# Performance work log

Hardware: AMD Instinct MI355X
Metric: run time of the kernel (lower is better)

## Reference

```python
import jax, jax.numpy as jnp
import numpy as np


def setup_inputs() -> dict:
    key = jax.random.key(0)
    k1, k2 = jax.random.split(key)
    # x: (N, width, T) with width == emb_width
    x = jax.random.normal(k1, (16, 64, 8192), dtype=jnp.float32)
    # codebook k: (k_bins, emb_width)
    k = jax.random.normal(k2, (2048, 64), dtype=jnp.float32) * 0.02
    return {"x": x, "k": k}


def reference(x, k):
    N, width, T = x.shape
    # preprocess: (N, width, T) -> (N*T, width)
    xf = jnp.transpose(x, (0, 2, 1)).reshape(-1, width)
    n_el = xf.size  # static python int
    prenorm = jnp.linalg.norm(xf - jnp.mean(xf)) / np.sqrt(n_el)
    # quantise: pairwise squared distances to codebook, argmin over codes
    # dist[i, j] = ||xf_i||^2 - 2 xf_i . k_j + ||k_j||^2   -> [NT, k_bins]
    dist = (jnp.sum(xf * xf, axis=-1, keepdims=True)
            - 2.0 * (xf @ k.T)
            + jnp.sum(k * k, axis=-1)[None, :])
    x_l = jnp.argmin(dist, axis=-1)          # [NT] codebook indices
    min_distance = jnp.min(dist, axis=-1)    # [NT]
    fit = jnp.mean(min_distance)
    # dequantise: embedding gather
    x_d = k[x_l]                              # [NT, width]
    # commit loss = ||detach(x_d) - x||^2 / numel
    commit_loss = jnp.sum((jax.lax.stop_gradient(x_d) - xf) ** 2) / n_el
    # straight-through estimator
    x_d = xf + jax.lax.stop_gradient(x_d - xf)
    # postprocess: back to (N, width, T) and (N, T)
    x_d = jnp.transpose(x_d.reshape(N, T, width), (0, 2, 1))
    x_l = x_l.reshape(N, T)
    return x_l, x_d, commit_loss, fit, prenorm
```

## Files before the change

### kernel.cpp

```cpp
#include <hip/hip_runtime.h>
#include <math.h>

#define WD 64
#define TD 8192
#define NT 131072
#define KB 2048
#define OFF_XL 0
#define OFF_XD NT
#define OFF_SC (NT + NT * WD)

#define CNT_OFF   32
#define KN2_OFF   4096
#define CB_OFF    16384
#define LIST_OFF  (16384 + 524288)
#define KT_OFF    (LIST_OFF + 4 * NT)
#define XR_OFF    (KT_OFF + 8 * NT)
#define FITV_OFF  (XR_OFF + XRCAP * WD * 4)
#define CMV_OFF   (FITV_OFF + 8 * NT)
#define PB_OFF    (CMV_OFF + 8 * NT)
#define XRCAP     32768

#define EPS_GAP 1e-3f
#define VEPS    2e-3f

typedef __attribute__((ext_vector_type(8))) short bf16x8_t;
typedef __attribute__((ext_vector_type(4))) float f32x4_t;

__device__ __forceinline__ unsigned short bf16_rne(float f) {
  unsigned int u = __float_as_uint(f);
  unsigned int r = u + 0x7fffu + ((u >> 16) & 1u);
  return (unsigned short)(r >> 16);
}

#define REP64(F) F(0) F(1) F(2) F(3) F(4) F(5) F(6) F(7) \
  F(8) F(9) F(10) F(11) F(12) F(13) F(14) F(15) \
  F(16) F(17) F(18) F(19) F(20) F(21) F(22) F(23) \
  F(24) F(25) F(26) F(27) F(28) F(29) F(30) F(31) \
  F(32) F(33) F(34) F(35) F(36) F(37) F(38) F(39) \
  F(40) F(41) F(42) F(43) F(44) F(45) F(46) F(47) \
  F(48) F(49) F(50) F(51) F(52) F(53) F(54) F(55) \
  F(56) F(57) F(58) F(59) F(60) F(61) F(62) F(63)

#define NP_SUMSQ64_NAMED(SVAR) \
  float r0 = __fmul_rn(x0, x0); \
  float r1 = __fmul_rn(x1, x1); \
  float r2 = __fmul_rn(x2, x2); \
  float r3 = __fmul_rn(x3, x3); \
  float r4 = __fmul_rn(x4, x4); \
  float r5 = __fmul_rn(x5, x5); \
  float r6 = __fmul_rn(x6, x6); \
  float r7 = __fmul_rn(x7, x7); \
  SQ8(8, 9, 10, 11, 12, 13, 14, 15) \
  SQ8(16, 17, 18, 19, 20, 21, 22, 23) \
  SQ8(24, 25, 26, 27, 28, 29, 30, 31) \
  SQ8(32, 33, 34, 35, 36, 37, 38, 39) \
  SQ8(40, 41, 42, 43, 44, 45, 46, 47) \
  SQ8(48, 49, 50, 51, 52, 53, 54, 55) \
  SQ8(56, 57, 58, 59, 60, 61, 62, 63) \
  const float SVAR = __fadd_rn(__fadd_rn(__fadd_rn(r0, r1), __fadd_rn(r2, r3)), \
                               __fadd_rn(__fadd_rn(r4, r5), __fadd_rn(r6, r7)));
#define SQ8(a,b,c,d,e,f,g,h) \
  r0 = __fadd_rn(r0, __fmul_rn(x##a, x##a)); \
  r1 = __fadd_rn(r1, __fmul_rn(x##b, x##b)); \
  r2 = __fadd_rn(r2, __fmul_rn(x##c, x##c)); \
  r3 = __fadd_rn(r3, __fmul_rn(x##d, x##d)); \
  r4 = __fadd_rn(r4, __fmul_rn(x##e, x##e)); \
  r5 = __fadd_rn(r5, __fmul_rn(x##f, x##f)); \
  r6 = __fadd_rn(r6, __fmul_rn(x##g, x##g)); \
  r7 = __fadd_rn(r7, __fmul_rn(x##h, x##h));

__device__ __forceinline__ float np_sumsq64_ptr(const float* a) {
  float r0 = __fmul_rn(a[0], a[0]);
  float r1 = __fmul_rn(a[1], a[1]);
  float r2 = __fmul_rn(a[2], a[2]);
  float r3 = __fmul_rn(a[3], a[3]);
  float r4 = __fmul_rn(a[4], a[4]);
  float r5 = __fmul_rn(a[5], a[5]);
  float r6 = __fmul_rn(a[6], a[6]);
  float r7 = __fmul_rn(a[7], a[7]);
#pragma unroll
  for (int i = 8; i < 64; i += 8) {
    r0 = __fadd_rn(r0, __fmul_rn(a[i + 0], a[i + 0]));
    r1 = __fadd_rn(r1, __fmul_rn(a[i + 1], a[i + 1]));
    r2 = __fadd_rn(r2, __fmul_rn(a[i + 2], a[i + 2]));
    r3 = __fadd_rn(r3, __fmul_rn(a[i + 3], a[i + 3]));
    r4 = __fadd_rn(r4, __fmul_rn(a[i + 4], a[i + 4]));
    r5 = __fadd_rn(r5, __fmul_rn(a[i + 5], a[i + 5]));
    r6 = __fadd_rn(r6, __fmul_rn(a[i + 6], a[i + 6]));
    r7 = __fadd_rn(r7, __fmul_rn(a[i + 7], a[i + 7]));
  }
  float t01 = __fadd_rn(r0, r1);
  float t23 = __fadd_rn(r2, r3);
  float t45 = __fadd_rn(r4, r5);
  float t67 = __fadd_rn(r6, r7);
  return __fadd_rn(__fadd_rn(t01, t23), __fadd_rn(t45, t67));
}

__global__ __launch_bounds__(256)
void vq_prep(const float* __restrict__ k, char* __restrict__ wsb) {
  int c = blockIdx.x * 256 + threadIdx.x;
  if (c >= KB) return;
  const float* kr = k + (size_t)c * WD;
  ((float*)(wsb + KN2_OFF))[c] = np_sumsq64_ptr(kr);
  float* kt = (float*)(wsb + KT_OFF);
#pragma unroll
  for (int w = 0; w < WD; ++w) kt[(size_t)w * KB + c] = kr[w];
  int jt = c >> 4, col = c & 15;
  unsigned short* cb = (unsigned short*)(wsb + CB_OFF);
#pragma unroll
  for (int w = 0; w < WD; ++w) {
    float f = kr[w];
    unsigned short hb = bf16_rne(f);
    float hf = __uint_as_float((unsigned int)hb << 16);
    unsigned short lb = bf16_rne(f - hf);
    int fH = w >> 5;
    int lane = col | (((w >> 3) & 3) << 4);
    int e = w & 7;
    cb[((size_t)((jt * 4 + fH) * 64 + lane)) * 8 + e] = hb;
    cb[((size_t)((jt * 4 + 2 + fH) * 64 + lane)) * 8 + e] = lb;
  }
}

__global__ __launch_bounds__(512) __attribute__((amdgpu_waves_per_eu(4)))
void vq_scan(const float* __restrict__ x, const float* __restrict__ k,
             float* __restrict__ out, char* __restrict__ wsb) {
  __shared__ float lkn2n[KB];
  __shared__ char cbuf[2][32768];
  __shared__ float sm1[256], sm2[256];
  __shared__ int sj1[256];
  __shared__ double sred[16];
  const int tid = threadIdx.x, lane = tid & 63, wave = tid >> 6;
  const int col = lane & 15, grp = lane >> 4;

  for (int i = tid; i < KB; i += 512)
    lkn2n[i] = -0.5f * ((const float*)(wsb + KN2_OFF))[i];

  const int n = blockIdx.x >> 5;
  const int t0 = (blockIdx.x & 31) * 256;
  const float* xb = x + (size_t)n * WD * TD;

  bf16x8_t aH[2][2], aL[2][2];
#pragma unroll
  for (int T = 0; T < 2; ++T) {
    const int trow = t0 + wave * 32 + T * 16 + col;
#pragma unroll
    for (int s = 0; s < 2; ++s) {
#pragma unroll
      for (int e = 0; e < 8; ++e) {
        int w = s * 32 + grp * 8 + e;
        float f = xb[(size_t)w * TD + trow];
        unsigned short hb = bf16_rne(f);
        float hf = __uint_as_float((unsigned int)hb << 16);
        unsigned short lb = bf16_rne(f - hf);
        aH[T][s][e] = (short)hb;
        aL[T][s][e] = (short)lb;
      }
    }
  }

  float M1[2][4], M2[2][4];
#pragma unroll
  for (int T = 0; T < 2; ++T)
#pragma unroll
    for (int e = 0; e < 4; ++e) {
      M1[T][e] = -INFINITY; M2[T][e] = -INFINITY;
    }

  const char* cbsrc = wsb + CB_OFF;
  float4 pf0, pf1, pf2, pf3;
#define PREF(c) { const float4* sp = (const float4*)(cbsrc + (size_t)(c) * 32768); \
    pf0 = sp[tid]; pf1 = sp[tid + 512]; pf2 = sp[tid + 1024]; pf3 = sp[tid + 1536]; }
#define WRBUF(b) { float4* dp = (float4*)cbuf[b]; \
    dp[tid] = pf0; dp[tid + 512] = pf1; dp[tid + 1024] = pf2; dp[tid + 1536] = pf3; }

  PREF(0)
  WRBUF(0)
  PREF(1)
  __syncthreads();

  for (int c = 0; c < 16; ++c) {
    const int cur = c & 1;
    if (c < 15) WRBUF(cur ^ 1)
    if (c < 14) PREF(c + 2)
#pragma unroll
    for (int jl = 0; jl < 8; ++jl) {
      const bf16x8_t* bp = (const bf16x8_t*)(cbuf[cur] + jl * 4096) + lane;
      bf16x8_t bH0 = bp[0], bH1 = bp[64], bL0 = bp[128], bL1 = bp[192];
      const int jt = c * 8 + jl;
      const float ci = lkn2n[jt * 16 + col];
#pragma unroll
      for (int T = 0; T < 2; ++T) {
        f32x4_t acc = {ci, ci, ci, ci};
        acc = __builtin_amdgcn_mfma_f32_16x16x32_bf16(aH[T][0], bH0, acc, 0, 0, 0);
        acc = __builtin_amdgcn_mfma_f32_16x16x32_bf16(aH[T][1], bH1, acc, 0, 0, 0);
        acc = __builtin_amdgcn_mfma_f32_16x16x32_bf16(aL[T][0], bH0, acc, 0, 0, 0);
        acc = __builtin_amdgcn_mfma_f32_16x16x32_bf16(aL[T][1], bH1, acc, 0, 0, 0);
        acc = __builtin_amdgcn_mfma_f32_16x16x32_bf16(aH[T][0], bL0, acc, 0, 0, 0);
        acc = __builtin_amdgcn_mfma_f32_16x16x32_bf16(aH[T][1], bL1, acc, 0, 0, 0);
#pragma unroll
        for (int e = 0; e < 4; ++e) {
          float vp = __uint_as_float(
              (__float_as_uint(acc[e]) & 0xFFFFFF80u) | (unsigned)jt);
          M2[T][e] = __builtin_amdgcn_fmed3f(M1[T][e], M2[T][e], vp);
          M1[T][e] = fmaxf(M1[T][e], vp);
        }
      }
    }
    __syncthreads();
  }
#undef PREF
#undef WRBUF

#pragma unroll
  for (int T = 0; T < 2; ++T)
#pragma unroll
    for (int e = 0; e < 4; ++e) {
      float m1 = M1[T][e], m2 = M2[T][e];
      int cd = (int)(__float_as_uint(m1) & 0x7Fu) * 16 + col;
#pragma unroll
      for (int d = 1; d < 16; d <<= 1) {
        float om1 = __shfl_xor(m1, d, 64);
        float om2 = __shfl_xor(m2, d, 64);
        int ocd = __shfl_xor(cd, d, 64);
        bool take = (om1 > m1) || (om1 == m1 && ocd < cd);
        float loser = take ? m1 : om1;
        m2 = fmaxf(fmaxf(m2, om2), loser);
        m1 = take ? om1 : m1;
        cd = take ? ocd : cd;
      }
      if (col == 0) {
        int r = wave * 32 + T * 16 + grp * 4 + e;
        sm1[r] = -2.f * m1;
        sm2[r] = -2.f * m2;
        sj1[r] = cd;
      }
    }
  __syncthreads();

  if (tid < 256) {
    const int row = blockIdx.x * 256 + tid;
    const int t = row & (TD - 1);
    const float m1r = sm1[tid], m2r = sm2[tid];
    const int j1r = sj1[tid];

    const float* xr = x + ((size_t)n * WD) * TD + t;
#define LOADX(w) float x##w = xr[(size_t)(w) * TD];
    REP64(LOADX)
#undef LOADX

    NP_SUMSQ64_NAMED(s)

    double xsum = 0.0, xsumsq = 0.0;
#define PRE(w) { double xd = (double)x##w; xsum += xd; xsumsq = fma(xd, xd, xsumsq); }
    REP64(PRE)
#undef PRE

    const float4* k4 = (const float4*)(k + (size_t)j1r * WD);
    float* xo = out + OFF_XD + ((size_t)n * WD) * TD + t;
    double commit = 0.0;
    float g = 0.f;
#define EPI1(w, KW) { \
      float kw = KW; \
      float diff = __fsub_rn(kw, x##w); \
      commit = fma((double)diff, (double)diff, commit); \
      g = __fmaf_rn(x##w, kw, g); \
      xo[(size_t)(w) * TD] = __fadd_rn(x##w, diff); }
    {
      float4 ka = k4[0], kb = k4[1], kc = k4[2], kd = k4[3];
      EPI1(0, ka.x) EPI1(1, ka.y) EPI1(2, ka.z) EPI1(3, ka.w)
      EPI1(4, kb.x) EPI1(5, kb.y) EPI1(6, kb.z) EPI1(7, kb.w)
      EPI1(8, kc.x) EPI1(9, kc.y) EPI1(10, kc.z) EPI1(11, kc.w)
      EPI1(12, kd.x) EPI1(13, kd.y) EPI1(14, kd.z) EPI1(15, kd.w)
    }
    {
      float4 ka = k4[4], kb = k4[5], kc = k4[6], kd = k4[7];
      EPI1(16, ka.x) EPI1(17, ka.y) EPI1(18, ka.z) EPI1(19, ka.w)
      EPI1(20, kb.x) EPI1(21, kb.y) EPI1(22, kb.z) EPI1(23, kb.w)
      EPI1(24, kc.x) EPI1(25, kc.y) EPI1(26, kc.z) EPI1(27, kc.w)
      EPI1(28, kd.x) EPI1(29, kd.y) EPI1(30, kd.z) EPI1(31, kd.w)
    }
    {
      float4 ka = k4[8], kb = k4[9], kc = k4[10], kd = k4[11];
      EPI1(32, ka.x) EPI1(33, ka.y) EPI1(34, ka.z) EPI1(35, ka.w)
      EPI1(36, kb.x) EPI1(37, kb.y) EPI1(38, kb.z) EPI1(39, kb.w)
      EPI1(40, kc.x) EPI1(41, kc.y) EPI1(42, kc.z) EPI1(43, kc.w)
      EPI1(44, kd.x) EPI1(45, kd.y) EPI1(46, kd.z) EPI1(47, kd.w)
    }
    {
      float4 ka = k4[12], kb = k4[13], kc = k4[14], kd = k4[15];
      EPI1(48, ka.x) EPI1(49, ka.y) EPI1(50, ka.z) EPI1(51, ka.w)
      EPI1(52, kb.x) EPI1(53, kb.y) EPI1(54, kb.z) EPI1(55, kb.w)
      EPI1(56, kc.x) EPI1(57, kc.y) EPI1(58, kc.z) EPI1(59, kc.w)
      EPI1(60, kd.x) EPI1(61, kd.y) EPI1(62, kd.z) EPI1(63, kd.w)
    }
#undef EPI1

    float kn2j = ((const float*)(wsb + KN2_OFF))[j1r];
    float score = kn2j - 2.f * g;
    bool resc = (m2r - m1r < EPS_GAP) || (fabsf(score - m1r) > VEPS);
    float dist1 = __fadd_rn(__fsub_rn(s, __fmul_rn(2.f, g)), kn2j);

    out[OFF_XL + row] = (float)j1r;
    if (resc) {
      unsigned idx = atomicAdd((unsigned*)(wsb + CNT_OFF), 1u);
      ((int*)(wsb + LIST_OFF))[idx] = row;
      if (idx < XRCAP) {
        float* xrw = (float*)(wsb + XR_OFF) + (size_t)idx * WD;
#define XWR(w) xrw[w] = x##w;
        REP64(XWR)
#undef XWR
      }
    }

    double v0 = xsum, v1 = xsumsq;
    double v2 = resc ? 0.0 : (double)dist1;
    double v3 = resc ? 0.0 : commit;
#pragma unroll
    for (int off = 32; off > 0; off >>= 1) {
      v0 += __shfl_down(v0, off, 64);
      v1 += __shfl_down(v1, off, 64);
      v2 += __shfl_down(v2, off, 64);
      v3 += __shfl_down(v3, off, 64);
    }
    if ((tid & 63) == 0) {
      int wv = tid >> 6;
      sred[wv * 4 + 0] = v0;
      sred[wv * 4 + 1] = v1;
      sred[wv * 4 + 2] = v2;
      sred[wv * 4 + 3] = v3;
    }
  }
  __syncthreads();
  if (tid == 0) {
    double a0 = 0, a1 = 0, a2 = 0, a3 = 0;
#pragma unroll
    for (int w2 = 0; w2 < 4; ++w2) {
      a0 += sred[w2 * 4 + 0];
      a1 += sred[w2 * 4 + 1];
      a2 += sred[w2 * 4 + 2];
      a3 += sred[w2 * 4 + 3];
    }
    double* pb = (double*)(wsb + PB_OFF) + (size_t)blockIdx.x * 4;
    pb[0] = a0; pb[1] = a1; pb[2] = a2; pb[3] = a3;
  }
}

__global__ __launch_bounds__(256)
void vq_rescan7(const float* __restrict__ x, const float* __restrict__ k,
                float* __restrict__ out, char* __restrict__ wsb) {
  __shared__ float xs[4][WD];
  __shared__ float ss[4];
  __shared__ unsigned long long wred[4][4];
  __shared__ unsigned long long bbest[4];
  const unsigned count = *(const unsigned*)(wsb + CNT_OFF);
  const int* list = (const int*)(wsb + LIST_OFF);
  const float* kn2 = (const float*)(wsb + KN2_OFF);
  const float* XR = (const float*)(wsb + XR_OFF);
  const float* kT = (const float*)(wsb + KT_OFF);
  double* fitv = (double*)(wsb + FITV_OFF);
  double* cmv = (double*)(wsb + CMV_OFF);
  const int tid = threadIdx.x;
  const int lane = tid & 63, wv = tid >> 6;
  const int c0 = tid * 8;

  for (unsigned base = blockIdx.x * 4u; base < count; base += gridDim.x * 4u) {
    __syncthreads();
    {
      const int r = tid >> 6, w = tid & 63;
      const unsigned li = base + (unsigned)r;
      if (li < count) {
        if (li < XRCAP) {
          xs[r][w] = XR[(size_t)li * WD + w];
        } else {
          const int row = list[li];
          const int n = row >> 13, t = row & (TD - 1);
          xs[r][w] = x[(size_t)n * WD * TD + (size_t)w * TD + t];
        }
      }
    }
    __syncthreads();
    if (lane == 0) ss[wv] = np_sumsq64_ptr(xs[wv]);
    __syncthreads();
    const float s0 = ss[0], s1 = ss[1], s2 = ss[2], s3 = ss[3];

    float a00 = 0.f, a01 = 0.f, a02 = 0.f, a03 = 0.f, a04 = 0.f, a05 = 0.f, a06 = 0.f, a07 = 0.f;
    float a10 = 0.f, a11 = 0.f, a12 = 0.f, a13 = 0.f, a14 = 0.f, a15 = 0.f, a16 = 0.f, a17 = 0.f;
    float a20 = 0.f, a21 = 0.f, a22 = 0.f, a23 = 0.f, a24 = 0.f, a25 = 0.f, a26 = 0.f, a27 = 0.f;
    float a30 = 0.f, a31 = 0.f, a32 = 0.f, a33 = 0.f, a34 = 0.f, a35 = 0.f, a36 = 0.f, a37 = 0.f;
    const float* kt = kT + c0;
#pragma unroll 4
    for (int w = 0; w < WD; ++w) {
      const float4 ka = *(const float4*)(kt + (size_t)w * KB);
      const float4 kb = *(const float4*)(kt + (size_t)w * KB + 4);
      const float xw0 = xs[0][w], xw1 = xs[1][w], xw2 = xs[2][w], xw3 = xs[3][w];
      a00 = __fmaf_rn(xw0, ka.x, a00); a01 = __fmaf_rn(xw0, ka.y, a01);
      a02 = __fmaf_rn(xw0, ka.z, a02); a03 = __fmaf_rn(xw0, ka.w, a03);
      a04 = __fmaf_rn(xw0, kb.x, a04); a05 = __fmaf_rn(xw0, kb.y, a05);
      a06 = __fmaf_rn(xw0, kb.z, a06); a07 = __fmaf_rn(xw0, kb.w, a07);
      a10 = __fmaf_rn(xw1, ka.x, a10); a11 = __fmaf_rn(xw1, ka.y, a11);
      a12 = __fmaf_rn(xw1, ka.z, a12); a13 = __fmaf_rn(xw1, ka.w, a13);
      a14 = __fmaf_rn(xw1, kb.x, a14); a15 = __fmaf_rn(xw1, kb.y, a15);
      a16 = __fmaf_rn(xw1, kb.z, a16); a17 = __fmaf_rn(xw1, kb.w, a17);
      a20 = __fmaf_rn(xw2, ka.x, a20); a21 = __fmaf_rn(xw2, ka.y, a21);
      a22 = __fmaf_rn(xw2, ka.z, a22); a23 = __fmaf_rn(xw2, ka.w, a23);
      a24 = __fmaf_rn(xw2, kb.x, a24); a25 = __fmaf_rn(xw2, kb.y, a25);
      a26 = __fmaf_rn(xw2, kb.z, a26); a27 = __fmaf_rn(xw2, kb.w, a27);
      a30 = __fmaf_rn(xw3, ka.x, a30); a31 = __fmaf_rn(xw3, ka.y, a31);
      a32 = __fmaf_rn(xw3, ka.z, a32); a33 = __fmaf_rn(xw3, ka.w, a33);
      a34 = __fmaf_rn(xw3, kb.x, a34); a35 = __fmaf_rn(xw3, kb.y, a35);
      a36 = __fmaf_rn(xw3, kb.z, a36); a37 = __fmaf_rn(xw3, kb.w, a37);
    }

#define ROWBEST(R, SV, A0, A1, A2, A3, A4, A5, A6, A7) { \
      unsigned long long best = ~0ull; \
      float d; unsigned long long p; \
      d = __fadd_rn(__fsub_rn(SV, __fmul_rn(2.f, A0)), kn2[c0 + 0]); \
      p = ((unsigned long long)__float_as_uint(d) << 32) | (unsigned)(c0 + 0); best = p < best ? p : best; \
      d = __fadd_rn(__fsub_rn(SV, __fmul_rn(2.f, A1)), kn2[c0 + 1]); \
      p = ((unsigned long long)__float_as_uint(d) << 32) | (unsigned)(c0 + 1); best = p < best ? p : best; \
      d = __fadd_rn(__fsub_rn(SV, __fmul_rn(2.f, A2)), kn2[c0 + 2]); \
      p = ((unsigned long long)__float_as_uint(d) << 32) | (unsigned)(c0 + 2); best = p < best ? p : best; \
      d = __fadd_rn(__fsub_rn(SV, __fmul_rn(2.f, A3)), kn2[c0 + 3]); \
      p = ((unsigned long long)__float_as_uint(d) << 32) | (unsigned)(c0 + 3); best = p < best ? p : best; \
      d = __fadd_rn(__fsub_rn(SV, __fmul_rn(2.f, A4)), kn2[c0 + 4]); \
      p = ((unsigned long long)__float_as_uint(d) << 32) | (unsigned)(c0 + 4); best = p < best ? p : best; \
      d = __fadd_rn(__fsub_rn(SV, __fmul_rn(2.f, A5)), kn2[c0 + 5]); \
      p = ((unsigned long long)__float_as_uint(d) << 32) | (unsigned)(c0 + 5); best = p < best ? p : best; \
      d = __fadd_rn(__fsub_rn(SV, __fmul_rn(2.f, A6)), kn2[c0 + 6]); \
      p = ((unsigned long long)__float_as_uint(d) << 32) | (unsigned)(c0 + 6); best = p < best ? p : best; \
      d = __fadd_rn(__fsub_rn(SV, __fmul_rn(2.f, A7)), kn2[c0 + 7]); \
      p = ((unsigned long long)__float_as_uint(d) << 32) | (unsigned)(c0 + 7); best = p < best ? p : best; \
      _Pragma("unroll") \
      for (int dd = 1; dd < 64; dd <<= 1) { \
        unsigned lo = (unsigned)best, hi = (unsigned)(best >> 32); \
        unsigned olo = __shfl_xor(lo, dd, 64); \
        unsigned ohi = __shfl_xor(hi, dd, 64); \
        unsigned long long o = ((unsigned long long)ohi << 32) | olo; \
        best = o < best ? o : best; \
      } \
      if (lane == 0) wred[R][wv] = best; }
    ROWBEST(0, s0, a00, a01, a02, a03, a04, a05, a06, a07)
    ROWBEST(1, s1, a10, a11, a12, a13, a14, a15, a16, a17)
    ROWBEST(2, s2, a20, a21, a22, a23, a24, a25, a26, a27)
    ROWBEST(3, s3, a30, a31, a32, a33, a34, a35, a36, a37)
#undef ROWBEST
    __syncthreads();
    if (tid < 4) {
      unsigned long long b = wred[tid][0];
      b = wred[tid][1] < b ? wred[tid][1] : b;
      b = wred[tid][2] < b ? wred[tid][2] : b;
      b = wred[tid][3] < b ? wred[tid][3] : b;
      bbest[tid] = b;
    }
    __syncthreads();

    {
      const int r = wv, w = lane;
      const unsigned li = base + (unsigned)r;
      if (li < count) {
        const int row = list[li];
        const int n = row >> 13, t = row & (TD - 1);
        const unsigned long long fb = bbest[r];
        const int bi = (int)(fb & 0xffffffffu);
        const float bv = __uint_as_float((unsigned)(fb >> 32));
        float kw = k[(size_t)bi * WD + w];
        float xw = xs[r][w];
        float diff = __fsub_rn(kw, xw);
        out[OFF_XD + (size_t)n * WD * TD + (size_t)w * TD + t] = __fadd_rn(xw, diff);
        double d2 = (double)diff * (double)diff;
#pragma unroll
        for (int dd = 32; dd > 0; dd >>= 1) d2 += __shfl_down(d2, dd, 64);
        if (w == 0) {
          out[OFF_XL + row] = (float)bi;
          fitv[li] = (double)bv;
          cmv[li] = d2;
        }
      }
    }
  }
}

__global__ __launch_bounds__(256)
void vq_final(const char* __restrict__ wsb, float* __restrict__ out) {
  __shared__ double sred[24];
  const unsigned count = *(const unsigned*)(wsb + CNT_OFF);
  const double* fitv = (const double*)(wsb + FITV_OFF);
  const double* cmv = (const double*)(wsb + CMV_OFF);
  const double* pb = (const double*)(wsb + PB_OFF);
  const int tid = threadIdx.x;

  double fa = 0.0, ca = 0.0;
  for (unsigned i = tid; i < count; i += 256) {
    fa += fitv[i];
    ca += cmv[i];
  }
  double b0 = 0.0, b1 = 0.0, b2 = 0.0, b3 = 0.0;
  for (int i = tid; i < 512; i += 256) {
    b0 += pb[i * 4 + 0];
    b1 += pb[i * 4 + 1];
    b2 += pb[i * 4 + 2];
    b3 += pb[i * 4 + 3];
  }
#pragma unroll
  for (int off = 32; off > 0; off >>= 1) {
    fa += __shfl_down(fa, off, 64);
    ca += __shfl_down(ca, off, 64);
    b0 += __shfl_down(b0, off, 64);
    b1 += __shfl_down(b1, off, 64);
    b2 += __shfl_down(b2, off, 64);
    b3 += __shfl_down(b3, off, 64);
  }
  if ((tid & 63) == 0) {
    int wv = tid >> 6;
    sred[wv * 6 + 0] = fa;
    sred[wv * 6 + 1] = ca;
    sred[wv * 6 + 2] = b0;
    sred[wv * 6 + 3] = b1;
    sred[wv * 6 + 4] = b2;
    sred[wv * 6 + 5] = b3;
  }
  __syncthreads();
  if (tid == 0) {
    double fit = 0, cm = 0, sum = 0, sumsq = 0;
#pragma unroll
    for (int i = 0; i < 4; ++i) {
      fit += sred[i * 6 + 0] + sred[i * 6 + 4];
      cm += sred[i * 6 + 1] + sred[i * 6 + 5];
      sum += sred[i * 6 + 2];
      sumsq += sred[i * 6 + 3];
    }
    double mean = sum / 8388608.0;
    double ss = sumsq - sum * mean;
    if (ss < 0.0) ss = 0.0;
    out[OFF_SC + 0] = (float)(cm / 8388608.0);
    out[OFF_SC + 1] = (float)(fit / 131072.0);
    out[OFF_SC + 2] = (float)sqrt(ss / 8388608.0);
  }
}

extern "C" void kernel_launch(void* const* d_in, const int* in_sizes, int n_in,
                              void* d_out, int out_size, void* d_ws, size_t ws_size,
                              hipStream_t stream) {
  const float* x = (const float*)d_in[0];
  const float* k = (const float*)d_in[1];
  float* out = (float*)d_out;
  char* wsb = (char*)d_ws;

  hipMemsetAsync(d_ws, 0, 64, stream);
  vq_prep<<<KB / 256, 256, 0, stream>>>(k, wsb);
  vq_scan<<<NT / 256, 512, 0, stream>>>(x, k, out, wsb);
  vq_rescan7<<<1024, 256, 0, stream>>>(x, k, out, wsb);
  vq_final<<<1, 256, 0, stream>>>(wsb, out);
}
```

Baseline: 159.4 us.

## Split epilogue across all 512 threads and drop compacted rescan row copy

The epilogue now runs on both halves of the block: each thread handles 32 of the 64 channels for one row, accumulating partial norms, dot products, sums and commit terms. The partials are exchanged through shared memory before a 256-thread finalization. The rescan kernel no longer gets a compacted copy of flagged rows and instead reloads them from x with strided gathers. This cuts per-thread register pressure and serial epilogue work, and removes the scattered row writes, at the cost of an extra barrier, shared-memory traffic and less coalesced rescan loads. The squared-norm sum also changes from a fixed 8-way tree to sequential FMA, so the fit values can differ slightly in rounding.

After: 159.2 us. No clear change (-0.1%).

```diff
diff --git a/kernel.cpp b/kernel.cpp
--- a/kernel.cpp
+++ b/kernel.cpp
@@ -14,11 +14,9 @@
 #define CB_OFF    16384
 #define LIST_OFF  (16384 + 524288)
 #define KT_OFF    (LIST_OFF + 4 * NT)
-#define XR_OFF    (KT_OFF + 8 * NT)
-#define FITV_OFF  (XR_OFF + XRCAP * WD * 4)
+#define FITV_OFF  (KT_OFF + 8 * NT)
 #define CMV_OFF   (FITV_OFF + 8 * NT)
 #define PB_OFF    (CMV_OFF + 8 * NT)
-#define XRCAP     32768
 
 #define EPS_GAP 1e-3f
 #define VEPS    2e-3f
@@ -32,42 +30,10 @@
   return (unsigned short)(r >> 16);
 }
 
-#define REP64(F) F(0) F(1) F(2) F(3) F(4) F(5) F(6) F(7) \
+#define REP32(F) F(0) F(1) F(2) F(3) F(4) F(5) F(6) F(7) \
   F(8) F(9) F(10) F(11) F(12) F(13) F(14) F(15) \
   F(16) F(17) F(18) F(19) F(20) F(21) F(22) F(23) \
-  F(24) F(25) F(26) F(27) F(28) F(29) F(30) F(31) \
-  F(32) F(33) F(34) F(35) F(36) F(37) F(38) F(39) \
-  F(40) F(41) F(42) F(43) F(44) F(45) F(46) F(47) \
-  F(48) F(49) F(50) F(51) F(52) F(53) F(54) F(55) \
-  F(56) F(57) F(58) F(59) F(60) F(61) F(62) F(63)
-
-#define NP_SUMSQ64_NAMED(SVAR) \
-  float r0 = __fmul_rn(x0, x0); \
-  float r1 = __fmul_rn(x1, x1); \
-  float r2 = __fmul_rn(x2, x2); \
-  float r3 = __fmul_rn(x3, x3); \
-  float r4 = __fmul_rn(x4, x4); \
-  float r5 = __fmul_rn(x5, x5); \
-  float r6 = __fmul_rn(x6, x6); \
-  float r7 = __fmul_rn(x7, x7); \
-  SQ8(8, 9, 10, 11, 12, 13, 14, 15) \
-  SQ8(16, 17, 18, 19, 20, 21, 22, 23) \
-  SQ8(24, 25, 26, 27, 28, 29, 30, 31) \
-  SQ8(32, 33, 34, 35, 36, 37, 38, 39) \
-  SQ8(40, 41, 42, 43, 44, 45, 46, 47) \
-  SQ8(48, 49, 50, 51, 52, 53, 54, 55) \
-  SQ8(56, 57, 58, 59, 60, 61, 62, 63) \
-  const float SVAR = __fadd_rn(__fadd_rn(__fadd_rn(r0, r1), __fadd_rn(r2, r3)), \
-                               __fadd_rn(__fadd_rn(r4, r5), __fadd_rn(r6, r7)));
-#define SQ8(a,b,c,d,e,f,g,h) \
-  r0 = __fadd_rn(r0, __fmul_rn(x##a, x##a)); \
-  r1 = __fadd_rn(r1, __fmul_rn(x##b, x##b)); \
-  r2 = __fadd_rn(r2, __fmul_rn(x##c, x##c)); \
-  r3 = __fadd_rn(r3, __fmul_rn(x##d, x##d)); \
-  r4 = __fadd_rn(r4, __fmul_rn(x##e, x##e)); \
-  r5 = __fadd_rn(r5, __fmul_rn(x##f, x##f)); \
-  r6 = __fadd_rn(r6, __fmul_rn(x##g, x##g)); \
-  r7 = __fadd_rn(r7, __fmul_rn(x##h, x##h));
+  F(24) F(25) F(26) F(27) F(28) F(29) F(30) F(31)
 
 __device__ __forceinline__ float np_sumsq64_ptr(const float* a) {
   float r0 = __fmul_rn(a[0], a[0]);
@@ -237,34 +203,36 @@
     }
   __syncthreads();
 
-  if (tid < 256) {
-    const int row = blockIdx.x * 256 + tid;
-    const int t = row & (TD - 1);
-    const float m1r = sm1[tid], m2r = sm2[tid];
-    const int j1r = sj1[tid];
-
-    const float* xr = x + ((size_t)n * WD) * TD + t;
-#define LOADX(w) float x##w = xr[(size_t)(w) * TD];
-    REP64(LOADX)
+  float* s_ex = (float*)cbuf[0];
+  float* g_ex = (float*)(cbuf[0] + 2048);
+  double* xs_ex = (double*)(cbuf[0] + 4096);
+  double* xq_ex = (double*)(cbuf[0] + 8192);
+  double* cm_ex = (double*)(cbuf[0] + 12288);
+
+  const int r = tid & 255, h = tid >> 8;
+  const int row = blockIdx.x * 256 + r;
+  const int t = row & (TD - 1);
+  const int j1r = sj1[r];
+  {
+    const float* xrh = x + ((size_t)n * WD + (size_t)h * 32) * TD + t;
+    float* xoh = out + OFF_XD + ((size_t)n * WD + (size_t)h * 32) * TD + t;
+    const float4* k4 = (const float4*)(k + (size_t)j1r * WD) + h * 8;
+
+#define LOADX(w) float x##w = xrh[(size_t)(w) * TD];
+    REP32(LOADX)
 #undef LOADX
 
-    NP_SUMSQ64_NAMED(s)
-
-    double xsum = 0.0, xsumsq = 0.0;
-#define PRE(w) { double xd = (double)x##w; xsum += xd; xsumsq = fma(xd, xd, xsumsq); }
-    REP64(PRE)
-#undef PRE
-
-    const float4* k4 = (const float4*)(k + (size_t)j1r * WD);
-    float* xo = out + OFF_XD + ((size_t)n * WD) * TD + t;
-    double commit = 0.0;
-    float g = 0.f;
+    float sp = 0.f, gp = 0.f;
+    double xsum = 0.0, xsumsq = 0.0, commit = 0.0;
 #define EPI1(w, KW) { \
       float kw = KW; \
+      sp = __fmaf_rn(x##w, x##w, sp); \
+      gp = __fmaf_rn(x##w, kw, gp); \
+      double xd = (double)x##w; \
+      xsum += xd; xsumsq = fma(xd, xd, xsumsq); \
       float diff = __fsub_rn(kw, x##w); \
       commit = fma((double)diff, (double)diff, commit); \
-      g = __fmaf_rn(x##w, kw, g); \
-      xo[(size_t)(w) * TD] = __fadd_rn(x##w, diff); }
+      xoh[(size_t)(w) * TD] = __fadd_rn(x##w, diff); }
     {
       float4 ka = k4[0], kb = k4[1], kc = k4[2], kd = k4[3];
       EPI1(0, ka.x) EPI1(1, ka.y) EPI1(2, ka.z) EPI1(3, ka.w)
@@ -279,37 +247,34 @@
       EPI1(24, kc.x) EPI1(25, kc.y) EPI1(26, kc.z) EPI1(27, kc.w)
       EPI1(28, kd.x) EPI1(29, kd.y) EPI1(30, kd.z) EPI1(31, kd.w)
     }
-    {
-      float4 ka = k4[8], kb = k4[9], kc = k4[10], kd = k4[11];
-      EPI1(32, ka.x) EPI1(33, ka.y) EPI1(34, ka.z) EPI1(35, ka.w)
-      EPI1(36, kb.x) EPI1(37, kb.y) EPI1(38, kb.z) EPI1(39, kb.w)
-      EPI1(40, kc.x) EPI1(41, kc.y) EPI1(42, kc.z) EPI1(43, kc.w)
-      EPI1(44, kd.x) EPI1(45, kd.y) EPI1(46, kd.z) EPI1(47, kd.w)
-    }
-    {
-      float4 ka = k4[12], kb = k4[13], kc = k4[14], kd = k4[15];
-      EPI1(48, ka.x) EPI1(49, ka.y) EPI1(50, ka.z) EPI1(51, ka.w)
-      EPI1(52, kb.x) EPI1(53, kb.y) EPI1(54, kb.z) EPI1(55, kb.w)
-      EPI1(56, kc.x) EPI1(57, kc.y) EPI1(58, kc.z) EPI1(59, kc.w)
-      EPI1(60, kd.x) EPI1(61, kd.y) EPI1(62, kd.z) EPI1(63, kd.w)
-    }
 #undef EPI1
 
-    float kn2j = ((const float*)(wsb + KN2_OFF))[j1r];
+    s_ex[h * 256 + r] = sp;
+    g_ex[h * 256 + r] = gp;
+    xs_ex[h * 256 + r] = xsum;
+    xq_ex[h * 256 + r] = xsumsq;
+    cm_ex[h * 256 + r] = commit;
+  }
+  __syncthreads();
+
+  if (tid < 256) {
+    const float m1r = sm1[tid], m2r = sm2[tid];
+    const float s = s_ex[tid] + s_ex[256 + tid];
+    const float g = g_ex[tid] + g_ex[256 + tid];
+    const double xsum = xs_ex[tid] + xs_ex[256 + tid];
+    const double xsumsq = xq_ex[tid] + xq_ex[256 + tid];
+    const double commit = cm_ex[tid] + cm_ex[256 + tid];
+    const int rowq = blockIdx.x * 256 + tid;
+
+    float kn2j = ((const float*)(wsb + KN2_OFF))[sj1[tid]];
     float score = kn2j - 2.f * g;
     bool resc = (m2r - m1r < EPS_GAP) || (fabsf(score - m1r) > VEPS);
-    float dist1 = __fadd_rn(__fsub_rn(s, __fmul_rn(2.f, g)), kn2j);
-
-    out[OFF_XL + row] = (float)j1r;
+    float dist1 = (s - 2.f * g) + kn2j;
+
+    out[OFF_XL + rowq] = (float)sj1[tid];
     if (resc) {
       unsigned idx = atomicAdd((unsigned*)(wsb + CNT_OFF), 1u);
-      ((int*)(wsb + LIST_OFF))[idx] = row;
-      if (idx < XRCAP) {
-        float* xrw = (float*)(wsb + XR_OFF) + (size_t)idx * WD;
-#define XWR(w) xrw[w] = x##w;
-        REP64(XWR)
-#undef XWR
-      }
+      ((int*)(wsb + LIST_OFF))[idx] = rowq;
     }
 
     double v0 = xsum, v1 = xsumsq;
@@ -355,7 +320,6 @@
   const unsigned count = *(const unsigned*)(wsb + CNT_OFF);
   const int* list = (const int*)(wsb + LIST_OFF);
   const float* kn2 = (const float*)(wsb + KN2_OFF);
-  const float* XR = (const float*)(wsb + XR_OFF);
   const float* kT = (const float*)(wsb + KT_OFF);
   double* fitv = (double*)(wsb + FITV_OFF);
   double* cmv = (double*)(wsb + CMV_OFF);
@@ -369,13 +333,9 @@
       const int r = tid >> 6, w = tid & 63;
       const unsigned li = base + (unsigned)r;
       if (li < count) {
-        if (li < XRCAP) {
-          xs[r][w] = XR[(size_t)li * WD + w];
-        } else {
-          const int row = list[li];
-          const int n = row >> 13, t = row & (TD - 1);
-          xs[r][w] = x[(size_t)n * WD * TD + (size_t)w * TD + t];
-        }
+        const int row = list[li];
+        const int n = row >> 13, t = row & (TD - 1);
+        xs[r][w] = x[(size_t)n * WD * TD + (size_t)w * TD + t];
       }
     }
     __syncthreads();
```
